# Optimization experiments

Hardware: AMD Instinct MI355X
Metric: run time of the kernel (lower is better)

Reference implementation:

```python
import jax, jax.numpy as jnp
import numpy as np

N_NODES = 50000
N_EDGES = 800000
IN_DIM = 128
HID = 128
HEADS = 4
OUT_DIM = 32
NEG_SLOPE = 0.2  # DGL GATConv default


def _gat_params(key, in_dim, out_feat, heads):
    k1, k2, k3 = jax.random.split(key, 3)
    s = 1.0 / np.sqrt(in_dim)
    W = jax.random.normal(k1, (in_dim, heads * out_feat), jnp.float32) * s
    attn_l = jax.random.normal(k2, (heads, out_feat), jnp.float32) * 0.1
    attn_r = jax.random.normal(k3, (heads, out_feat), jnp.float32) * 0.1
    b = jnp.zeros((heads * out_feat,), jnp.float32)
    return W, attn_l, attn_r, b


def setup_inputs() -> dict:
    key = jax.random.key(0)
    ks = jax.random.split(key, 10)
    inp = {
        "x_am": jax.random.normal(ks[0], (N_NODES, IN_DIM), jnp.float32),
        "x_ph": jax.random.normal(ks[1], (N_NODES, IN_DIM), jnp.float32),
        "exist": jax.random.uniform(ks[2], (N_EDGES,), jnp.float32),
        "am_exist": jax.random.uniform(ks[3], (N_EDGES,), jnp.float32),
        "src": jax.random.randint(ks[4], (N_EDGES,), 0, N_NODES, jnp.int32),
        "dst": jax.random.randint(ks[5], (N_EDGES,), 0, N_NODES, jnp.int32),
    }
    # layer 0 (input_dim -> hidden//head per head), layer 1 (hidden -> output_dim per head)
    inp["W0a"], inp["al0a"], inp["ar0a"], inp["b0a"] = _gat_params(ks[6], IN_DIM, HID // HEADS, HEADS)
    inp["W0p"], inp["al0p"], inp["ar0p"], inp["b0p"] = _gat_params(ks[7], IN_DIM, HID // HEADS, HEADS)
    inp["W1a"], inp["al1a"], inp["ar1a"], inp["b1a"] = _gat_params(ks[8], HID, OUT_DIM, HEADS)
    inp["W1p"], inp["al1p"], inp["ar1p"], inp["b1p"] = _gat_params(ks[9], HID, OUT_DIM, HEADS)
    return inp


def gat_conv(x, src, dst, W, attn_l, attn_r, b, edge_w, n_nodes):
    """DGL-style GATConv with edge_weight: out[i] = sum_{e: dst=i} softmax_i(LeakyReLU(el[src]+er[dst])) * w_e * ft[src]."""
    heads, outf = attn_l.shape
    ft = (x @ W).reshape(-1, heads, outf)                 # (N, H, F)
    el = jnp.sum(ft * attn_l, axis=-1)                    # (N, H)
    er = jnp.sum(ft * attn_r, axis=-1)                    # (N, H)
    e = jax.nn.leaky_relu(el[src] + er[dst], NEG_SLOPE)   # (E, H)
    emax = jax.ops.segment_max(e, dst, num_segments=n_nodes)
    emax = jnp.where(jnp.isfinite(emax), emax, 0.0)       # guard isolated nodes
    ex = jnp.exp(e - emax[dst])
    denom = jax.ops.segment_sum(ex, dst, num_segments=n_nodes)
    a = ex / jnp.maximum(denom[dst], 1e-9)                # edge softmax over incoming edges
    a = a * edge_w[:, None]                               # post-softmax edge weighting
    out = jax.ops.segment_sum(ft[src] * a[:, :, None], dst, num_segments=n_nodes)  # (N, H, F)
    return out + b.reshape(heads, outf)


def reference(x_am, x_ph, exist, am_exist,
              W0a, al0a, ar0a, b0a, W0p, al0p, ar0p, b0p,
              W1a, al1a, ar1a, b1a, W1p, al1p, ar1p, b1p,
              src, dst):
    n = x_am.shape[0]
    # layer 0: GATConv -> flatten -> ReLU (dropout rate 0 in eval)
    h_am = gat_conv(x_am, src, dst, W0a, al0a, ar0a, b0a, am_exist, n)
    h_ph = gat_conv(x_ph, src, dst, W0p, al0p, ar0p, b0p, exist, n)
    h_am = jax.nn.relu(h_am.reshape(n, -1))
    h_ph = jax.nn.relu(h_ph.reshape(n, -1))
    # layer 1 (last): GATConv -> mean over heads
    h_am = gat_conv(h_am, src, dst, W1a, al1a, ar1a, b1a, am_exist, n).mean(axis=1)
    h_ph = gat_conv(h_ph, src, dst, W1p, al1p, ar1p, b1p, exist, n).mean(axis=1)
    return (h_am, h_ph)
```

## Files before the change

### kernel.cpp

```cpp
#include <hip/hip_runtime.h>
#include <hip/hip_fp16.h>


typedef _Float16 f16x8 __attribute__((ext_vector_type(8)));
typedef float f32x4 __attribute__((ext_vector_type(4)));

struct GemmP { const void* X; const __half* Wt; const float *al, *ar; __half* Y; float *el, *er; };
struct ChP   { const __half* ft; const float *el, *er, *bias; void* out; };

__global__ void hist_wprep_kernel(const int* __restrict__ dst, int* __restrict__ counts, int E,
                                  const float* __restrict__ W0a, const float* __restrict__ W0p,
                                  const float* __restrict__ W1a, const float* __restrict__ W1p,
                                  __half* __restrict__ Wt) {
  int e = blockIdx.x * blockDim.x + threadIdx.x;
  if (e < E) atomicAdd(&counts[dst[e]], 1);
  if (e < 65536) {
    int m = e >> 14, i = e & 16383;
    const float* W = (m == 0) ? W0a : (m == 1) ? W0p : (m == 2) ? W1a : W1p;
    int nn = i >> 7, k = i & 127;
    Wt[(size_t)m * 16384 + nn * 128 + k] = __float2half_rn(W[k * 128 + nn]);
  }
}

__global__ __launch_bounds__(256) void scan_kernel(const int* __restrict__ counts,
                                                   int* __restrict__ offsets,
                                                   int* __restrict__ cursor,
                                                   int* __restrict__ sync,
                                                   int nb_stride, int n, int E) {
  __shared__ int lds[256];
  __shared__ int sbid, sprev;
  int* state = sync + 64;
  int* agg = state + nb_stride;
  int* incl = agg + nb_stride;
  int t = threadIdx.x;
  if (t == 0) sbid = atomicAdd(sync, 1);
  __syncthreads();
  int bid = sbid;
  int i = bid * 256 + t;
  int v = (i < n) ? counts[i] : 0;
  lds[t] = v;
  __syncthreads();
  for (int off = 1; off < 256; off <<= 1) {
    int x = (t >= off) ? lds[t - off] : 0;
    __syncthreads();
    lds[t] += x;
    __syncthreads();
  }
  int total = lds[255];
  if (t == 0) {
    if (bid == 0) {
      __hip_atomic_store(&incl[0], total, __ATOMIC_RELAXED, __HIP_MEMORY_SCOPE_AGENT);
      __hip_atomic_store(&state[0], 2, __ATOMIC_RELEASE, __HIP_MEMORY_SCOPE_AGENT);
      sprev = 0;
    } else {
      __hip_atomic_store(&agg[bid], total, __ATOMIC_RELAXED, __HIP_MEMORY_SCOPE_AGENT);
      __hip_atomic_store(&state[bid], 1, __ATOMIC_RELEASE, __HIP_MEMORY_SCOPE_AGENT);
    }
  }
  if (bid > 0 && t < 64) {
    int run = 0;
    int base = bid - 1;
    while (true) {
      int idx = base - t;
      int st = 2, val = 0;
      if (idx >= 0) {
        do {
          st = __hip_atomic_load(&state[idx], __ATOMIC_ACQUIRE, __HIP_MEMORY_SCOPE_AGENT);
        } while (st == 0);
        val = (st == 2)
                  ? __hip_atomic_load(&incl[idx], __ATOMIC_RELAXED, __HIP_MEMORY_SCOPE_AGENT)
                  : __hip_atomic_load(&agg[idx], __ATOMIC_RELAXED, __HIP_MEMORY_SCOPE_AGENT);
      }
      unsigned long long done = __ballot(st == 2);
      int firstDone = (int)__ffsll(done) - 1;
      int contrib = (firstDone < 0) ? val : ((t <= firstDone) ? val : 0);
#pragma unroll
      for (int o = 1; o < 64; o <<= 1) contrib += __shfl_xor(contrib, o);
      run += contrib;
      if (firstDone >= 0) break;
      base -= 64;
    }
    if (t == 0) {
      __hip_atomic_store(&incl[bid], run + total, __ATOMIC_RELAXED, __HIP_MEMORY_SCOPE_AGENT);
      __hip_atomic_store(&state[bid], 2, __ATOMIC_RELEASE, __HIP_MEMORY_SCOPE_AGENT);
      sprev = run;
    }
  }
  __syncthreads();
  int prev = sprev;
  if (i < n) {
    int off = prev + lds[t] - v;
    offsets[i] = off;
    cursor[i] = off;
  }
  if (i == 0) offsets[n] = E;
}

__global__ void fill_kernel(const int* __restrict__ src, const int* __restrict__ dst,
                            const float* __restrict__ exist, const float* __restrict__ am_exist,
                            int* __restrict__ cursor, int4* __restrict__ edge16, int E) {
  int e = blockIdx.x * blockDim.x + threadIdx.x;
  if (e >= E) return;
  int d = dst[e];
  int pos = atomicAdd(&cursor[d], 1);
  edge16[pos] = make_int4(src[e], d, __float_as_int(am_exist[e]), __float_as_int(exist[e]));
}

template <int AFP16>
__global__ __launch_bounds__(256) void gemm_kernel(GemmP p0, GemmP p1, int n) {
  GemmP p = blockIdx.y ? p1 : p0;
  constexpr int LDH = 72;
  constexpr int LDE = 136;
  __shared__ __half lds[2 * 128 * LDH];
  __half* As = lds;
  __half* Ws = lds + 128 * LDH;
  int t = threadIdx.x;
  int row0 = blockIdx.x << 7;
  int wv = t >> 6, lane = t & 63;
  int m = lane & 15, q = lane >> 4;

  f32x4 acc[2][8];
#pragma unroll
  for (int rt = 0; rt < 2; ++rt)
#pragma unroll
    for (int ct = 0; ct < 8; ++ct) acc[rt][ct] = (f32x4){0.f, 0.f, 0.f, 0.f};

#pragma unroll
  for (int kh = 0; kh < 2; ++kh) {
    __syncthreads();
    if (AFP16) {
      const __half* Xh = (const __half*)p.X;
#pragma unroll
      for (int i = 0; i < 4; ++i) {
        int c = t + (i << 8);
        int r = c >> 3, o8 = c & 7;
        uint4 v = make_uint4(0, 0, 0, 0);
        if (row0 + r < n)
          v = *(const uint4*)(Xh + (size_t)(row0 + r) * 128 + (kh << 6) + (o8 << 3));
        *(uint4*)(As + r * LDH + (o8 << 3)) = v;
      }
    } else {
      const float* Xf = (const float*)p.X;
#pragma unroll
      for (int i = 0; i < 8; ++i) {
        int c = t + (i << 8);
        int r = c >> 4, f4 = c & 15;
        float4 v = make_float4(0.f, 0.f, 0.f, 0.f);
        if (row0 + r < n)
          v = *(const float4*)(Xf + (size_t)(row0 + r) * 128 + (kh << 6) + (f4 << 2));
        union { __half h[4]; uint2 u; } pk;
        pk.h[0] = __float2half_rn(v.x); pk.h[1] = __float2half_rn(v.y);
        pk.h[2] = __float2half_rn(v.z); pk.h[3] = __float2half_rn(v.w);
        *(uint2*)(As + r * LDH + (f4 << 2)) = pk.u;
      }
    }
#pragma unroll
    for (int i = 0; i < 4; ++i) {
      int c = t + (i << 8);
      int r = c >> 3, o8 = c & 7;
      uint4 v = *(const uint4*)(p.Wt + (size_t)r * 128 + (kh << 6) + (o8 << 3));
      *(uint4*)(Ws + r * LDH + (o8 << 3)) = v;
    }
    __syncthreads();
#pragma unroll
    for (int kc = 0; kc < 2; ++kc) {
      f16x8 a0 = *(const f16x8*)(As + (wv * 32 + m) * LDH + kc * 32 + q * 8);
      f16x8 a1 = *(const f16x8*)(As + (wv * 32 + 16 + m) * LDH + kc * 32 + q * 8);
#pragma unroll
      for (int ct = 0; ct < 8; ++ct) {
        f16x8 b = *(const f16x8*)(Ws + (ct * 16 + m) * LDH + kc * 32 + q * 8);
        acc[0][ct] = __builtin_amdgcn_mfma_f32_16x16x32_f16(a0, b, acc[0][ct], 0, 0, 0);
        acc[1][ct] = __builtin_amdgcn_mfma_f32_16x16x32_f16(a1, b, acc[1][ct], 0, 0, 0);
      }
    }
  }
  __syncthreads();
#pragma unroll
  for (int rt = 0; rt < 2; ++rt) {
    int rbase = wv * 32 + rt * 16 + q * 4;
#pragma unroll
    for (int ct = 0; ct < 8; ++ct) {
      int col = ct * 16 + m;
#pragma unroll
      for (int r = 0; r < 4; ++r)
        lds[(rbase + r) * LDE + col] = __float2half_rn(acc[rt][ct][r]);
    }
  }
  __syncthreads();
  {
    int r = t & 127;
    int half = t >> 7;
    int row = row0 + r;
    if (row < n) {
      float e0 = 0.f, e1 = 0.f, r0 = 0.f, r1 = 0.f;
#pragma unroll
      for (int i = 0; i < 8; ++i) {
        int cbase = half * 64 + i * 8;
        f16x8 v = *(const f16x8*)(lds + r * LDE + cbase);
        *(uint4*)(p.Y + (size_t)row * 128 + cbase) = *(const uint4*)&v;
#pragma unroll
        for (int j = 0; j < 8; ++j) {
          float f = (float)v[j];
          float av = p.al[cbase + j];
          float rv = p.ar[cbase + j];
          if (((i * 8 + j) >> 5) == 0) { e0 = fmaf(f, av, e0); r0 = fmaf(f, rv, r0); }
          else                         { e1 = fmaf(f, av, e1); r1 = fmaf(f, rv, r1); }
        }
      }
      *(float2*)(p.el + (size_t)row * 4 + half * 2) = make_float2(e0, e1);
      *(float2*)(p.er + (size_t)row * 4 + half * 2) = make_float2(r0, r1);
    }
  }
}

template <int LAYER>
__global__ __launch_bounds__(256) void gather_kernel(ChP c0, ChP c1,
                                                     const int* __restrict__ offs,
                                                     const int4* __restrict__ edge16, int n) {
  int t = threadIdx.x;
  int w = t >> 6;
  int lane = t & 63;
  int node = blockIdx.x * 2 + (w >> 1);
  int ch = w & 1;
  if (node >= n) return;
  ChP P = ch ? c1 : c0;
  int hh = lane >> 4;
  int ce = lane & 7;

  int start = __builtin_amdgcn_readfirstlane(offs[node]);
  int end = __builtin_amdgcn_readfirstlane(offs[node + 1]);
  float er_h = P.er[(size_t)node * 4 + hh];
  const __half2* ftbase = (const __half2*)P.ft;
  const float* elb = P.el;
  const int* e32 = (const int*)edge16;

  float acc0 = 0.f, acc1 = 0.f, l = 0.f;
  int k = start;
  while (k + 8 <= end) {
    int4 ed[8];
#pragma unroll
    for (int j = 0; j < 8; ++j) ed[j] = edge16[k + j];
    int s_v = e32[(size_t)(k + ce) * 4];
    float el_v = elb[(size_t)s_v * 4 + hh];
    float ev = el_v + er_h;
    ev = (ev > 0.f) ? ev : 0.2f * ev;
    float x_v = __expf(ev);
#pragma unroll
    for (int j = 0; j < 8; ++j) {
      int s = ed[j].x;
      float wgt = __int_as_float(ch ? ed[j].w : ed[j].z);
      __half2 fh = ftbase[(size_t)s * 64 + lane];
      float x = __shfl(x_v, j, 16);
      l += x;
      float cv = x * wgt;
      acc0 = fmaf(cv, __low2float(fh), acc0);
      acc1 = fmaf(cv, __high2float(fh), acc1);
    }
    k += 8;
  }
  for (; k < end; ++k) {
    int4 ed = edge16[k];
    int s = ed.x;
    float wgt = __int_as_float(ch ? ed.w : ed.z);
    float el_s = elb[(size_t)s * 4 + hh];
    float ev = el_s + er_h;
    ev = (ev > 0.f) ? ev : 0.2f * ev;
    float x = __expf(ev);
    __half2 fh = ftbase[(size_t)s * 64 + lane];
    l += x;
    float cv = x * wgt;
    acc0 = fmaf(cv, __low2float(fh), acc0);
    acc1 = fmaf(cv, __high2float(fh), acc1);
  }

  float rl = 1.f / fmaxf(l, 1e-9f);
  float2 b2 = *(const float2*)(P.bias + lane * 2);
  float v0 = fmaf(acc0, rl, b2.x);
  float v1 = fmaf(acc1, rl, b2.y);
  if (LAYER == 0) {
    __half2 h = __floats2half2_rn(fmaxf(v0, 0.f), fmaxf(v1, 0.f));
    ((__half2*)P.out)[(size_t)node * 64 + lane] = h;
  } else {
    v0 += __shfl_xor(v0, 16); v1 += __shfl_xor(v1, 16);
    v0 += __shfl_xor(v0, 32); v1 += __shfl_xor(v1, 32);
    if (lane < 16) {
      *(float2*)((float*)P.out + (size_t)node * 32 + lane * 2) =
          make_float2(0.25f * v0, 0.25f * v1);
    }
  }
}

extern "C" void kernel_launch(void* const* d_in, const int* in_sizes, int n_in,
                              void* d_out, int out_size, void* d_ws, size_t ws_size,
                              hipStream_t stream) {
  const float* x_am = (const float*)d_in[0];
  const float* x_ph = (const float*)d_in[1];
  const float* exist = (const float*)d_in[2];
  const float* am_exist = (const float*)d_in[3];
  const int* src = (const int*)d_in[4];
  const int* dst = (const int*)d_in[5];
  const float* W0a = (const float*)d_in[6];
  const float* al0a = (const float*)d_in[7];
  const float* ar0a = (const float*)d_in[8];
  const float* b0a = (const float*)d_in[9];
  const float* W0p = (const float*)d_in[10];
  const float* al0p = (const float*)d_in[11];
  const float* ar0p = (const float*)d_in[12];
  const float* b0p = (const float*)d_in[13];
  const float* W1a = (const float*)d_in[14];
  const float* al1a = (const float*)d_in[15];
  const float* ar1a = (const float*)d_in[16];
  const float* b1a = (const float*)d_in[17];
  const float* W1p = (const float*)d_in[18];
  const float* al1p = (const float*)d_in[19];
  const float* ar1p = (const float*)d_in[20];
  const float* b1p = (const float*)d_in[21];

  int n = in_sizes[0] / 128;
  int E = in_sizes[2];
  int N_pad = (n + 255) & ~255;
  int nb = (n + 255) / 256;
  int NB_pad = (nb + 63) & ~63;

  size_t szN = (size_t)N_pad * 4;
  size_t szSync = (size_t)(64 + 3 * NB_pad) * 4;
  size_t szOffs = (size_t)(N_pad + 8) * 4;
  size_t szE16 = (size_t)E * 16;
  size_t szFt16 = (size_t)n * 128 * 2;
  size_t szEl = (size_t)N_pad * 4 * 4;
  size_t szWt = (size_t)4 * 128 * 128 * 2;

  auto rnd = [](size_t b) { return (b + 255) & ~(size_t)255; };
  size_t fixed = 2 * rnd(szN) + rnd(szSync) + rnd(szOffs) + rnd(szE16) +
                 4 * rnd(szEl) + rnd(szWt);
  bool dual = ws_size >= fixed + 4 * rnd(szFt16);

  char* p = (char*)d_ws;
  auto take = [&](size_t b) { char* q = p; p += (b + 255) & ~(size_t)255; return q; };
  int* counts = (int*)take(szN);
  int* sync = (int*)take(szSync);
  int* cursor = (int*)take(szN);
  int* offs = (int*)take(szOffs);
  int4* edge16 = (int4*)take(szE16);
  __half* Wt = (__half*)take(szWt);
  float* el_am = (float*)take(szEl);
  float* el_ph = (float*)take(szEl);
  float* er_am = (float*)take(szEl);
  float* er_ph = (float*)take(szEl);
  __half* ft_am = (__half*)take(szFt16);
  __half* ft_ph = dual ? (__half*)take(szFt16) : ft_am;
  __half* hb_am = (__half*)take(szFt16);
  __half* hb_ph = dual ? (__half*)take(szFt16) : hb_am;

  float* out_am = (float*)d_out;
  float* out_ph = out_am + (size_t)n * 32;

  (void)hipMemsetAsync(counts, 0, rnd(szN) + rnd(szSync), stream);
  hist_wprep_kernel<<<(E + 255) / 256, 256, 0, stream>>>(dst, counts, E,
                                                         W0a, W0p, W1a, W1p, Wt);
  scan_kernel<<<nb, 256, 0, stream>>>(counts, offs, cursor, sync, NB_pad, n, E);
  fill_kernel<<<(E + 255) / 256, 256, 0, stream>>>(src, dst, exist, am_exist,
                                                   cursor, edge16, E);

  int gg = (n + 127) / 128;
  int gw = (n + 1) / 2;
  GemmP g0a{x_am, Wt,          al0a, ar0a, ft_am, el_am, er_am};
  GemmP g0p{x_ph, Wt + 16384,  al0p, ar0p, ft_ph, el_ph, er_ph};
  GemmP g1a{hb_am, Wt + 32768, al1a, ar1a, ft_am, el_am, er_am};
  GemmP g1p{hb_ph, Wt + 49152, al1p, ar1p, ft_ph, el_ph, er_ph};
  ChP c0a{ft_am, el_am, er_am, b0a, hb_am};
  ChP c0p{ft_ph, el_ph, er_ph, b0p, hb_ph};
  ChP c1a{ft_am, el_am, er_am, b1a, out_am};
  ChP c1p{ft_ph, el_ph, er_ph, b1p, out_ph};

  if (dual) {
    gemm_kernel<0><<<dim3(gg, 2), 256, 0, stream>>>(g0a, g0p, n);
    gather_kernel<0><<<gw, 256, 0, stream>>>(c0a, c0p, offs, edge16, n);
    gemm_kernel<1><<<dim3(gg, 2), 256, 0, stream>>>(g1a, g1p, n);
    gather_kernel<1><<<gw, 256, 0, stream>>>(c1a, c1p, offs, edge16, n);
  } else {
    gemm_kernel<0><<<dim3(gg, 2), 256, 0, stream>>>(g0a, g0a, n);
    gather_kernel<0><<<gw, 256, 0, stream>>>(c0a, c0a, offs, edge16, n);
    gemm_kernel<1><<<dim3(gg, 2), 256, 0, stream>>>(g1a, g1a, n);
    gather_kernel<1><<<gw, 256, 0, stream>>>(c1a, c1a, offs, edge16, n);
    gemm_kernel<0><<<dim3(gg, 2), 256, 0, stream>>>(g0p, g0p, n);
    gather_kernel<0><<<gw, 256, 0, stream>>>(c0p, c0p, offs, edge16, n);
    gemm_kernel<1><<<dim3(gg, 2), 256, 0, stream>>>(g1p, g1p, n);
    gather_kernel<1><<<gw, 256, 0, stream>>>(c1p, c1p, offs, edge16, n);
  }
}
```

Before: 435.1 us.

## Co-schedule CSR edge fill with layer-0 GEMM in one launch

Merges the edge-fill scatter and the layer-0 projection GEMM into a single kernel, where the first 256 blocks run a grid-stride fill loop and the remaining blocks run the GEMM tiles. Both stages are independent, so the latency-bound atomic scatter can overlap with the compute-heavy GEMM and one launch boundary is removed. The cost is that the fill now uses fewer blocks with grid-striding, and the GEMM blocks share CU resources with the fill blocks, which can lengthen the fill's critical path.

```diff
diff --git a/kernel.cpp b/kernel.cpp
--- a/kernel.cpp
+++ b/kernel.cpp
@@ -96,26 +96,35 @@
   if (i == 0) offsets[n] = E;
 }
 
+__device__ __forceinline__ void fill_edges(int b0, int nfb,
+                                           const int* __restrict__ src,
+                                           const int* __restrict__ dst,
+                                           const float* __restrict__ exist,
+                                           const float* __restrict__ am_exist,
+                                           int* __restrict__ cursor,
+                                           int4* __restrict__ edge16, int E) {
+  for (int e = b0 * 256 + threadIdx.x; e < E; e += nfb * 256) {
+    int d = dst[e];
+    int pos = atomicAdd(&cursor[d], 1);
+    edge16[pos] = make_int4(src[e], d, __float_as_int(am_exist[e]), __float_as_int(exist[e]));
+  }
+}
+
 __global__ void fill_kernel(const int* __restrict__ src, const int* __restrict__ dst,
                             const float* __restrict__ exist, const float* __restrict__ am_exist,
                             int* __restrict__ cursor, int4* __restrict__ edge16, int E) {
-  int e = blockIdx.x * blockDim.x + threadIdx.x;
-  if (e >= E) return;
-  int d = dst[e];
-  int pos = atomicAdd(&cursor[d], 1);
-  edge16[pos] = make_int4(src[e], d, __float_as_int(am_exist[e]), __float_as_int(exist[e]));
+  fill_edges(blockIdx.x, gridDim.x, src, dst, exist, am_exist, cursor, edge16, E);
 }
 
 template <int AFP16>
-__global__ __launch_bounds__(256) void gemm_kernel(GemmP p0, GemmP p1, int n) {
-  GemmP p = blockIdx.y ? p1 : p0;
+__device__ __forceinline__ void gemm_body(GemmP p, int bx, int n) {
   constexpr int LDH = 72;
   constexpr int LDE = 136;
   __shared__ __half lds[2 * 128 * LDH];
   __half* As = lds;
   __half* Ws = lds + 128 * LDH;
   int t = threadIdx.x;
-  int row0 = blockIdx.x << 7;
+  int row0 = bx << 7;
   int wv = t >> 6, lane = t & 63;
   int m = lane & 15, q = lane >> 4;
 
@@ -211,6 +220,25 @@
       *(float2*)(p.er + (size_t)row * 4 + half * 2) = make_float2(r0, r1);
     }
   }
+}
+
+template <int AFP16>
+__global__ __launch_bounds__(256) void gemm_kernel(GemmP p0, GemmP p1, int n) {
+  gemm_body<AFP16>(blockIdx.y ? p1 : p0, blockIdx.x, n);
+}
+
+__global__ __launch_bounds__(256) void fill_gemm0_kernel(
+    GemmP p0, GemmP p1, int gg, int n, int nfb,
+    const int* __restrict__ src, const int* __restrict__ dst,
+    const float* __restrict__ exist, const float* __restrict__ am_exist,
+    int* __restrict__ cursor, int4* __restrict__ edge16, int E) {
+  int b = blockIdx.x;
+  if (b < nfb) {
+    fill_edges(b, nfb, src, dst, exist, am_exist, cursor, edge16, E);
+    return;
+  }
+  int g = b - nfb;
+  gemm_body<0>((g >= gg) ? p1 : p0, (g >= gg) ? g - gg : g, n);
 }
 
 template <int LAYER>
@@ -359,8 +387,6 @@
   hist_wprep_kernel<<<(E + 255) / 256, 256, 0, stream>>>(dst, counts, E,
                                                          W0a, W0p, W1a, W1p, Wt);
   scan_kernel<<<nb, 256, 0, stream>>>(counts, offs, cursor, sync, NB_pad, n, E);
-  fill_kernel<<<(E + 255) / 256, 256, 0, stream>>>(src, dst, exist, am_exist,
-                                                   cursor, edge16, E);
 
   int gg = (n + 127) / 128;
   int gw = (n + 1) / 2;
@@ -374,11 +400,15 @@
   ChP c1p{ft_ph, el_ph, er_ph, b1p, out_ph};
 
   if (dual) {
-    gemm_kernel<0><<<dim3(gg, 2), 256, 0, stream>>>(g0a, g0p, n);
+    constexpr int NFB = 256;
+    fill_gemm0_kernel<<<NFB + 2 * gg, 256, 0, stream>>>(
+        g0a, g0p, gg, n, NFB, src, dst, exist, am_exist, cursor, edge16, E);
     gather_kernel<0><<<gw, 256, 0, stream>>>(c0a, c0p, offs, edge16, n);
     gemm_kernel<1><<<dim3(gg, 2), 256, 0, stream>>>(g1a, g1p, n);
     gather_kernel<1><<<gw, 256, 0, stream>>>(c1a, c1p, offs, edge16, n);
   } else {
+    fill_kernel<<<(E + 255) / 256, 256, 0, stream>>>(src, dst, exist, am_exist,
+                                                     cursor, edge16, E);
     gemm_kernel<0><<<dim3(gg, 2), 256, 0, stream>>>(g0a, g0a, n);
     gather_kernel<0><<<gw, 256, 0, stream>>>(c0a, c0a, offs, edge16, n);
     gemm_kernel<1><<<dim3(gg, 2), 256, 0, stream>>>(g1a, g1a, n);
```

New measurement: 410.2 us. 5.7% less time.
